# Optimization experiments

Hardware: AMD Instinct MI355X
Metric: run time of the kernel (lower is better)

## Reference

```python
import jax, jax.numpy as jnp
import numpy as np

NL, D, Di, N, R, K, V, NH = 24, 768, 1536, 16, 48, 4, 50280, 12
BATCH, SEQ = 4, 256


def setup_inputs():
    key = jax.random.key(0)
    it = iter(jax.random.split(key, 48))
    g = lambda shape, s=0.02: jax.random.normal(next(it), shape, jnp.float32) * s
    inp = {
        "question_ids": jax.random.randint(next(it), (BATCH, SEQ), 0, V),
        "question_mask": jnp.ones((BATCH, SEQ), jnp.int32),
        "answer_ids": jax.random.randint(next(it), (BATCH, SEQ), 0, V),
        "answer_mask": jnp.ones((BATCH, SEQ), jnp.int32),
        "embed": g((V, D)),
        "norm_w": jnp.ones((NL, D)),
        "in_proj_w": g((NL, 2 * Di, D)),
        "conv_w": g((NL, Di, K), 0.1),
        "conv_b": jnp.zeros((NL, Di)),
        "x_proj_w": g((NL, R + 2 * N, Di)),
        "dt_proj_w": g((NL, Di, R)),
        "dt_proj_b": g((NL, Di), 0.5) - 4.0,
        "A_log": jnp.log(jnp.broadcast_to(jnp.arange(1, N + 1, dtype=jnp.float32), (NL, Di, N))) + 0.0,
        "D_p": jnp.ones((NL, Di)),
        "out_proj_w": g((NL, D, Di)),
        "norm_f": jnp.ones((D,)),
        "ln1_w": jnp.ones((D,)), "ln1_b": jnp.zeros((D,)),
        "qkv_w": g((3 * D, D)), "qkv_b": jnp.zeros((3 * D,)),
        "attn_out_w": g((D, D)), "attn_out_b": jnp.zeros((D,)),
        "ln2_w": jnp.ones((D,)), "ln2_b": jnp.zeros((D,)),
        "ff1_w": g((4 * D, D)), "ff1_b": jnp.zeros((4 * D,)),
        "ff2_w": g((D, 4 * D)), "ff2_b": jnp.zeros((D,)),
        "C_w": g((1, N)), "proj_out_w": g((D, Di)),
        "B_w": g((N, 1)), "proj_in_w": g((Di, D), 0.002),
    }
    return inp


def _rms(x, w, eps=1e-5):
    return x * jax.lax.rsqrt(jnp.mean(x * x, axis=-1, keepdims=True) + eps) * w


def _ln(x, w, b, eps=1e-5):
    m = jnp.mean(x, axis=-1, keepdims=True)
    v = jnp.var(x, axis=-1, keepdims=True)
    return (x - m) * jax.lax.rsqrt(v + eps) * w + b


def _mamba_block(h, layer, init_state):
    nw, ipw, cw, cb, xpw, dpw, dpb, alog, dp, opw = layer
    x_in = _rms(h, nw)
    xz = jnp.einsum('bld,ed->ble', x_in, ipw)  # (B,L,2*Di)
    x, z = jnp.split(xz, 2, axis=-1)
    L = x.shape[1]
    xp = jnp.pad(x, ((0, 0), (K - 1, 0), (0, 0)))  # causal depthwise conv, kernel K
    x = sum(xp[:, k:k + L, :] * cw[:, k] for k in range(K)) + cb
    x = jax.nn.silu(x)
    dbl = jnp.einsum('bld,ed->ble', x, xpw)
    dt, Bm, Cm = dbl[..., :R], dbl[..., R:R + N], dbl[..., R + N:]
    delta = jax.nn.softplus(jnp.einsum('blr,dr->bld', dt, dpw) + dpb)  # (B,L,Di)
    A = -jnp.exp(alog)  # (Di,N)

    def step(hs, t):  # selective scan, carry (B,Di,N)
        d_t, x_t, B_t, C_t = t
        hs = jnp.exp(d_t[..., None] * A) * hs + (d_t * x_t)[..., None] * B_t[:, None, :]
        return hs, jnp.einsum('bdn,bn->bd', hs, C_t)

    xs = tuple(jnp.moveaxis(a, 1, 0) for a in (delta, x, Bm, Cm))
    last, ys = jax.lax.scan(step, init_state, xs)
    y = jnp.moveaxis(ys, 0, 1) + x * dp
    y = y * jax.nn.silu(z)
    return h + jnp.einsum('bld,od->blo', y, opw), last


def _backbone(ids, mask, embed, mamba_params, norm_f, init_states):
    h = embed[ids] * mask[..., None].astype(embed.dtype)
    block = jax.checkpoint(_mamba_block)  # remat per layer: bounds bwd memory

    def layer_step(carry, xs):
        *layer, st = xs
        return block(carry, tuple(layer), st)

    h, lasts = jax.lax.scan(layer_step, h, mamba_params + (init_states,))
    h = _rms(h, norm_f)
    return jnp.einsum('bld,vd->blv', h, embed), lasts  # tied lm head


def _tf_layer(x, ln1_w, ln1_b, qkv_w, qkv_b, attn_out_w, attn_out_b, ln2_w, ln2_b, ff1_w, ff1_b, ff2_w, ff2_b):
    B, S, _ = x.shape
    hd = D // NH
    y = _ln(x, ln1_w, ln1_b)  # norm_first pre-LN
    q, k, v = jnp.split(y @ qkv_w.T + qkv_b, 3, axis=-1)
    q = q.reshape(B, S, NH, hd); k = k.reshape(B, S, NH, hd); v = v.reshape(B, S, NH, hd)
    att = jax.nn.softmax(jnp.einsum('bqhd,bkhd->bhqk', q, k) / jnp.sqrt(jnp.float32(hd)), axis=-1)
    o = jnp.einsum('bhqk,bkhd->bqhd', att, v).reshape(B, S, D)
    x = x + o @ attn_out_w.T + attn_out_b
    y = _ln(x, ln2_w, ln2_b)
    return x + jax.nn.gelu(y @ ff1_w.T + ff1_b, approximate=False) @ ff2_w.T + ff2_b


def _refine(states, C_w, proj_out_w, B_w, proj_in_w, tf_params):
    # states: (B, NL, Di, N); 12-step recurrent state refinement
    for _ in range(12):
        d = jnp.einsum('bsdn,n->bsd', states, C_w[0])  # C: Linear(16,1), squeeze(-1)
        d = jnp.einsum('bsd,od->bso', d, proj_out_w)   # 1536 -> 768
        d = _tf_layer(d, *tf_params)
        d = jnp.einsum('bso,do->bsd', d, proj_in_w)    # 768 -> 1536
        states = states + d[..., None] * B_w[:, 0]     # B: Linear(1,16)
    return states


def reference(question_ids, question_mask, answer_ids, answer_mask, embed, norm_w, in_proj_w, conv_w, conv_b, x_proj_w, dt_proj_w, dt_proj_b, A_log, D_p, out_proj_w, norm_f, ln1_w, ln1_b, qkv_w, qkv_b, attn_out_w, attn_out_b, ln2_w, ln2_b, ff1_w, ff1_b, ff2_w, ff2_b, C_w, proj_out_w, B_w, proj_in_w):
    mamba_params = (norm_w, in_proj_w, conv_w, conv_b, x_proj_w, dt_proj_w, dt_proj_b, A_log, D_p, out_proj_w)
    tf_params = (ln1_w, ln1_b, qkv_w, qkv_b, attn_out_w, attn_out_b, ln2_w, ln2_b, ff1_w, ff1_b, ff2_w, ff2_b)
    Bsz = question_ids.shape[0]
    zeros = jnp.zeros((NL, Bsz, Di, N), embed.dtype)
    _, lasts = _backbone(question_ids, question_mask, embed, mamba_params, norm_f, zeros)
    states = jnp.moveaxis(lasts, 0, 1)  # torch.stack(states, dim=1): (B, NL, Di, N)
    states = _refine(states, C_w, proj_out_w, B_w, proj_in_w, tf_params)
    logits, _ = _backbone(answer_ids, answer_mask, embed, mamba_params, norm_f, jnp.moveaxis(states, 0, 1))
    return logits
```

## Files before the change

kernel.cpp:

```cpp
#include <hip/hip_runtime.h>
#include <math.h>

namespace {

constexpr int kNL = 24, kD = 768, kDi = 1536, kN = 16, kR = 48, kK = 4, kV = 50280, kNH = 12;
constexpr int kB = 4, kS = 256;
constexpr int kMtok = kB * kS;
constexpr int kMref = kB * kNL;
constexpr int kVp = 50304;
constexpr int kNx = 1568;
constexpr int kNxPad = 1600;

using bf16x8 = __attribute__((ext_vector_type(8))) short;
using f32x4  = __attribute__((ext_vector_type(4))) float;

__device__ __forceinline__ float siluf(float x) { return x / (1.f + __expf(-x)); }

__device__ __forceinline__ ushort f2b(float f) {
    union { float f; unsigned u; } v; v.f = f;
    unsigned u = v.u;
    unsigned r = (u + 0x7FFFu + ((u >> 16) & 1u)) >> 16;
    return (ushort)r;
}

#define GLOAD_LDS(g, l) \
    __builtin_amdgcn_global_load_lds((const __attribute__((address_space(1))) void*)(g), \
                                     (__attribute__((address_space(3))) void*)(l), 16, 0, 0)

template <int BM, int BN, int BIAS, int ACT, int RES, int OUTMODE, int PIPE>
__global__ __launch_bounds__(256, (PIPE == 3 ? 3 : 2)) void gemm_bf16(
    const ushort* __restrict__ A, int lda,
    const ushort* __restrict__ B, int ldb,
    float* __restrict__ C, int ldc,
    ushort* __restrict__ Cbf, int ldcb,
    float* __restrict__ C2,
    const float* __restrict__ bias,
    const float* __restrict__ aux,
    int M, int N, int K)
{
    constexpr int ACH = BM / 32;
    constexpr int BCH = BN / 32;
    constexpr int MI  = BM / 32;
    constexpr int NJ  = BN / 32;

    __shared__ ushort As[PIPE][BM * 64];
    __shared__ ushort Bs[PIPE][BN * 64];

    const int tid  = threadIdx.x;
    const int lane = tid & 63;
    const int wave = tid >> 6;
    const int m0 = blockIdx.y * BM;
    const int n0 = blockIdx.x * BN;
    const int wr = (wave >> 1) * (BM / 2);
    const int wc = (wave & 1) * (BN / 2);

    f32x4 acc[MI][NJ];
#pragma unroll
    for (int i = 0; i < MI; ++i)
#pragma unroll
        for (int j = 0; j < NJ; ++j) acc[i][j] = f32x4{0.f, 0.f, 0.f, 0.f};

    const int srow = lane >> 3;
    const int scol = ((lane & 7) ^ srow) * 8;
    const ushort* gA[ACH];
    const ushort* gB[BCH];
#pragma unroll
    for (int g = 0; g < ACH; ++g)
        gA[g] = A + (size_t)(m0 + (g * 4 + wave) * 8 + srow) * lda + scol;
#pragma unroll
    for (int g = 0; g < BCH; ++g)
        gB[g] = B + (size_t)(n0 + (g * 4 + wave) * 8 + srow) * ldb + scol;

    const int frow = lane & 15;
    const int kh   = lane >> 4;
    const int nt   = K >> 6;

    auto stage = [&](int t, int buf) {
        const int off = t * 64;
#pragma unroll
        for (int g = 0; g < ACH; ++g) GLOAD_LDS(gA[g] + off, &As[buf][(g * 4 + wave) * 512]);
#pragma unroll
        for (int g = 0; g < BCH; ++g) GLOAD_LDS(gB[g] + off, &Bs[buf][(g * 4 + wave) * 512]);
    };
    auto compute = [&](int buf) {
#pragma unroll
        for (int s = 0; s < 2; ++s) {
            bf16x8 fa[MI], fb[NJ];
#pragma unroll
            for (int i = 0; i < MI; ++i) {
                int r = wr + i * 16 + frow;
                int slot = (s * 4 + kh) ^ (r & 7);
                fa[i] = *(const bf16x8*)&As[buf][r * 64 + slot * 8];
            }
#pragma unroll
            for (int j = 0; j < NJ; ++j) {
                int r = wc + j * 16 + frow;
                int slot = (s * 4 + kh) ^ (r & 7);
                fb[j] = *(const bf16x8*)&Bs[buf][r * 64 + slot * 8];
            }
#pragma unroll
            for (int i = 0; i < MI; ++i)
#pragma unroll
                for (int j = 0; j < NJ; ++j)
                    acc[i][j] = __builtin_amdgcn_mfma_f32_16x16x32_bf16(fa[i], fb[j], acc[i][j], 0, 0, 0);
        }
    };

    if constexpr (PIPE == 3) {
        stage(0, 0);
        if (nt > 1) stage(1, 1);
        for (int t = 0; t < nt; ++t) {
            if (t < nt - 1) {
                asm volatile("s_waitcnt vmcnt(%0)" :: "n"(ACH + BCH) : "memory");
            } else {
                asm volatile("s_waitcnt vmcnt(0)" ::: "memory");
            }
            __builtin_amdgcn_s_barrier();
            if (t + 2 < nt) stage(t + 2, (t + 2) % 3);
            compute(t % 3);
        }
        __builtin_amdgcn_s_barrier();
    } else {
        stage(0, 0);
        __syncthreads();
        int cur = 0;
        for (int t = 0; t < nt; ++t) {
            if (t + 1 < nt) stage(t + 1, cur ^ 1);
            compute(cur);
            __syncthreads();
            cur ^= 1;
        }
    }

    const int ccol = lane & 15;
    const int crow = (lane >> 4) * 4;
#pragma unroll
    for (int i = 0; i < MI; ++i) {
#pragma unroll
        for (int j = 0; j < NJ; ++j) {
            int gn = n0 + wc + j * 16 + ccol;
            if (gn >= N) continue;
            float bv = BIAS ? bias[gn] : 0.f;
#pragma unroll
            for (int q = 0; q < 4; ++q) {
                int gm = m0 + wr + i * 16 + crow + q;
                if (gm >= M) continue;
                float v = acc[i][j][q] + bv;
                if (ACT == 1) v = fmaxf(v, 0.f) + log1pf(expf(-fabsf(v)));
                if (ACT == 2) v = 0.5f * v * (1.f + erff(v * 0.70710678118654752f));
                if (OUTMODE == 5) {
                    if (gn < kDi) C[(size_t)gm * kDi + gn] = v;
                    else C2[(size_t)(gn - kDi) * kMtok + gm] = siluf(v);
                } else if (OUTMODE == 6) {
                    if (gn < 32) C2[(size_t)gn * kMtok + gm] = v;
                    else {
                        float w = v + bias[gn - 32];
                        w = fmaxf(w, 0.f) + log1pf(expf(-fabsf(w)));
                        C[(size_t)(gn - 32) * kMtok + gm] = w;
                    }
                } else if (OUTMODE == 7) {
                    int bb = gm / kNL, ss = gm - bb * kNL;
                    float* stp = C2 + ((size_t)(ss * kB + bb) * kDi + gn) * kN;
                    float a2 = 0.f;
#pragma unroll
                    for (int nn = 0; nn < kN; ++nn) {
                        float sv = stp[nn] + v * bias[nn];
                        stp[nn] = sv;
                        a2 += sv * aux[nn];
                    }
                    Cbf[(size_t)gm * ldcb + gn] = f2b(a2);
                } else {
                    size_t ci = (size_t)gm * ldc + gn;
                    if (RES) v += C[ci];
                    if (OUTMODE != 2) C[ci] = v;
                    if (OUTMODE == 1 || OUTMODE == 2) Cbf[(size_t)gm * ldcb + gn] = f2b(v);
                }
            }
        }
    }
}

template <int BM, int BN, int BIAS, int ACT, int RES, int OUTMODE, int PIPE>
static void gemm(const ushort* A, int lda, const ushort* B, int ldb,
                 float* C, int ldc, ushort* Cb, int ldcb, float* C2,
                 const float* bias, const float* aux, int M, int N, int K, hipStream_t s)
{
    dim3 g((N + BN - 1) / BN, (M + BM - 1) / BM);
    gemm_bf16<BM, BN, BIAS, ACT, RES, OUTMODE, PIPE><<<g, dim3(256), 0, s>>>(
        A, lda, B, ldb, C, ldc, Cb, ldcb, C2, bias, aux, M, N, K);
}

__global__ void cvt_kernel(const float* __restrict__ src, ushort* __restrict__ dst, int n) {
    int i = (blockIdx.x * 256 + threadIdx.x) * 4;
    if (i >= n) return;
    float4 v = *(const float4*)(src + i);
    ushort4 o; o.x = f2b(v.x); o.y = f2b(v.y); o.z = f2b(v.z); o.w = f2b(v.w);
    *(ushort4*)(dst + i) = o;
}

__global__ void cvt_dpw_kernel(const float* __restrict__ src, ushort* __restrict__ dst) {
    int i = blockIdx.x * 256 + threadIdx.x;
    if (i >= 24 * 1536 * 64) return;
    int col = i & 63, row = i >> 6;
    dst[i] = (col < 48) ? f2b(src[(size_t)row * 48 + col]) : (ushort)0;
}

__global__ void cvt_xpwdtT_kernel(const float* __restrict__ src, ushort* __restrict__ dst) {
    int i = blockIdx.x * 256 + threadIdx.x;
    if (i >= 24 * 1536 * 64) return;
    int r = i & 63;
    int j = (i >> 6) % 1536;
    int l = i / (1536 * 64);
    dst[i] = (r < 48) ? f2b(src[((size_t)l * 80 + r) * 1536 + j]) : (ushort)0;
}

__global__ void cvt_bc_kernel(const float* __restrict__ src, ushort* __restrict__ dst) {
    int i = blockIdx.x * 256 + threadIdx.x;
    if (i >= 24 * 32 * 1536) return;
    int k = i % 1536;
    int gn = (i / 1536) % 32;
    int l = i / (32 * 1536);
    dst[((size_t)l * kNxPad + gn) * 1536 + k] = f2b(src[((size_t)l * 80 + 48 + gn) * 1536 + k]);
}

__global__ void embed_kernel(const int* __restrict__ ids, const int* __restrict__ msk,
                             const float* __restrict__ embed, float* __restrict__ h)
{
    int i = blockIdx.x * 256 + threadIdx.x;
    int row = i / kD, col = i - row * kD;
    h[i] = embed[(size_t)ids[row] * kD + col] * (float)msk[row];
}

__global__ __launch_bounds__(256) void rms_kernel(const float* __restrict__ x,
                                                  const float* __restrict__ w,
                                                  ushort* __restrict__ out)
{
    __shared__ float red[256];
    int row = blockIdx.x, tid = threadIdx.x;
    const float* xr = x + (size_t)row * kD;
    float s = 0.f;
    for (int j = tid; j < kD; j += 256) { float v = xr[j]; s += v * v; }
    red[tid] = s; __syncthreads();
    for (int o = 128; o > 0; o >>= 1) { if (tid < o) red[tid] += red[tid + o]; __syncthreads(); }
    float rs = rsqrtf(red[0] / (float)kD + 1e-5f);
    for (int j = tid; j < kD; j += 256) out[(size_t)row * kD + j] = f2b(xr[j] * rs * w[j]);
}

__global__ __launch_bounds__(256) void ln_kernel(const float* __restrict__ x,
                                                 const float* __restrict__ w,
                                                 const float* __restrict__ b,
                                                 ushort* __restrict__ out)
{
    __shared__ float r1[256], r2[256];
    int row = blockIdx.x, tid = threadIdx.x;
    const float* xr = x + (size_t)row * kD;
    float s = 0.f, s2 = 0.f;
    for (int j = tid; j < kD; j += 256) { float v = xr[j]; s += v; s2 += v * v; }
    r1[tid] = s; r2[tid] = s2; __syncthreads();
    for (int o = 128; o > 0; o >>= 1) {
        if (tid < o) { r1[tid] += r1[tid + o]; r2[tid] += r2[tid + o]; }
        __syncthreads();
    }
    float mean = r1[0] / (float)kD;
    float var = r2[0] / (float)kD - mean * mean;
    float rs = rsqrtf(var + 1e-5f);
    for (int j = tid; j < kD; j += 256)
        out[(size_t)row * kD + j] = f2b((xr[j] - mean) * rs * w[j] + b[j]);
}

__global__ __launch_bounds__(256) void conv_kernel(
    const float* __restrict__ xbuf, const float* __restrict__ cw,
    const float* __restrict__ cb, ushort* __restrict__ xc_bf,
    float* __restrict__ xcT)
{
    int d   = blockIdx.x * 256 + threadIdx.x;
    int bt0 = blockIdx.y * 16;
    int t0  = bt0 & (kS - 1);
    float w0 = cw[d * 4], w1 = cw[d * 4 + 1], w2 = cw[d * 4 + 2], w3 = cw[d * 4 + 3];
    float bias = cb[d];
    float xv[19];
#pragma unroll
    for (int j = 0; j < 19; ++j) {
        int tt = t0 - 3 + j;
        xv[j] = (tt >= 0) ? xbuf[(size_t)(bt0 - 3 + j) * kDi + d] : 0.f;
    }
    float out[16];
#pragma unroll
    for (int e = 0; e < 16; ++e) {
        float s = bias + xv[e] * w0 + xv[e + 1] * w1 + xv[e + 2] * w2 + xv[e + 3] * w3;
        float v = siluf(s);
        out[e] = v;
        xc_bf[(size_t)(bt0 + e) * kDi + d] = f2b(v);
    }
    float4* dst = (float4*)(xcT + (size_t)d * kMtok + bt0);
#pragma unroll
    for (int i = 0; i < 4; ++i)
        dst[i] = make_float4(out[i * 4], out[i * 4 + 1], out[i * 4 + 2], out[i * 4 + 3]);
}

__global__ __launch_bounds__(256) void scan_kernel(
    const float* __restrict__ dltT, const float* __restrict__ xcT,
    const float* __restrict__ zT, const float* __restrict__ bcT,
    const float* __restrict__ alog, const float* __restrict__ dp,
    float* __restrict__ states, ushort* __restrict__ y)
{
    int gid = blockIdx.x * 256 + threadIdx.x;
    int n = gid & 15;
    int d = (gid >> 4) % kDi;
    int b = gid / (kDi * kN);
    float Areg = -__expf(alog[d * kN + n]);
    float dpv = dp[d];
    size_t sidx = (size_t)(b * kDi + d) * kN + n;
    float hs = states[sidx];
    const float4* pD = (const float4*)(dltT + (size_t)d * kMtok + b * kS);
    const float4* pX = (const float4*)(xcT  + (size_t)d * kMtok + b * kS);
    const float4* pZ = (const float4*)(zT   + (size_t)d * kMtok + b * kS);
    const float4* pB = (const float4*)(bcT + (size_t)n * kMtok + b * kS);
    const float4* pC = (const float4*)(bcT + (size_t)(16 + n) * kMtok + b * kS);
    float4 D = pD[0], X = pX[0], Z = pZ[0], Bq = pB[0], Cq = pC[0];
    ushort* yrow = y + (size_t)(b * kS) * kDi + d;
    for (int g = 0; g < kS / 4; ++g) {
        float4 Dn, Xn, Zn, Bn, Cn;
        if (g + 1 < kS / 4) { Dn = pD[g + 1]; Xn = pX[g + 1]; Zn = pZ[g + 1]; Bn = pB[g + 1]; Cn = pC[g + 1]; }
#pragma unroll
        for (int e = 0; e < 4; ++e) {
            float dv = (&D.x)[e], xv = (&X.x)[e], zv = (&Z.x)[e];
            float Bv = (&Bq.x)[e], Cv = (&Cq.x)[e];
            hs = __expf(dv * Areg) * hs + (dv * xv) * Bv;
            float p = hs * Cv;
            p += __shfl_xor(p, 1, 16);
            p += __shfl_xor(p, 2, 16);
            p += __shfl_xor(p, 4, 16);
            p += __shfl_xor(p, 8, 16);
            if (n == 0) yrow[(size_t)(g * 4 + e) * kDi] = f2b((p + xv * dpv) * zv);
        }
        D = Dn; X = Xn; Z = Zn; Bq = Bn; Cq = Cn;
    }
    states[sidx] = hs;
}

__global__ void contract_kernel(const float* __restrict__ st, const float* __restrict__ Cw,
                                ushort* __restrict__ dDi)
{
    int i = blockIdx.x * 256 + threadIdx.x;
    int row = i / kDi, di = i - row * kDi;
    int b = row / kNL, s = row - b * kNL;
    const float* sp = st + ((size_t)(s * kB + b) * kDi + di) * kN;
    float acc = 0.f;
#pragma unroll
    for (int nn = 0; nn < kN; ++nn) acc += sp[nn] * Cw[nn];
    dDi[i] = f2b(acc);
}

__global__ __launch_bounds__(32) void attn_kernel(const float* __restrict__ qkv,
                                                  ushort* __restrict__ o)
{
    int b = blockIdx.x / kNH;
    int hh = blockIdx.x - b * kNH;
    int sq = threadIdx.x;
    if (sq >= kNL) return;
    const float* qrow = qkv + (size_t)(b * kNL + sq) * (3 * kD) + hh * 64;
    float q[64];
#pragma unroll
    for (int e = 0; e < 64; ++e) q[e] = qrow[e];
    float sc[kNL];
    float mx = -1e30f;
    for (int sk = 0; sk < kNL; ++sk) {
        const float* krow = qkv + (size_t)(b * kNL + sk) * (3 * kD) + kD + hh * 64;
        float dt = 0.f;
#pragma unroll
        for (int e = 0; e < 64; ++e) dt += q[e] * krow[e];
        dt *= 0.125f;
        sc[sk] = dt;
        mx = fmaxf(mx, dt);
    }
    float sum = 0.f;
    for (int sk = 0; sk < kNL; ++sk) { sc[sk] = expf(sc[sk] - mx); sum += sc[sk]; }
    float inv = 1.f / sum;
    float out[64];
#pragma unroll
    for (int e = 0; e < 64; ++e) out[e] = 0.f;
    for (int sk = 0; sk < kNL; ++sk) {
        float wgt = sc[sk] * inv;
        const float* vrow = qkv + (size_t)(b * kNL + sk) * (3 * kD) + 2 * kD + hh * 64;
#pragma unroll
        for (int e = 0; e < 64; ++e) out[e] += wgt * vrow[e];
    }
    ushort* orow = o + (size_t)(b * kNL + sq) * kD + hh * 64;
#pragma unroll
    for (int e = 0; e < 64; ++e) orow[e] = f2b(out[e]);
}

}

extern "C" void kernel_launch(void* const* d_in, const int* in_sizes, int n_in,
                              void* d_out, int out_size, void* d_ws, size_t ws_size,
                              hipStream_t stream)
{
    const int*   q_ids  = (const int*)d_in[0];
    const int*   q_msk  = (const int*)d_in[1];
    const int*   a_ids  = (const int*)d_in[2];
    const int*   a_msk  = (const int*)d_in[3];
    const float* embed  = (const float*)d_in[4];
    const float* norm_w = (const float*)d_in[5];
    const float* ipw    = (const float*)d_in[6];
    const float* cw     = (const float*)d_in[7];
    const float* cb     = (const float*)d_in[8];
    const float* xpw    = (const float*)d_in[9];
    const float* dpw    = (const float*)d_in[10];
    const float* dpb    = (const float*)d_in[11];
    const float* alog   = (const float*)d_in[12];
    const float* dpp    = (const float*)d_in[13];
    const float* opw    = (const float*)d_in[14];
    const float* norm_f = (const float*)d_in[15];
    const float* ln1w   = (const float*)d_in[16];
    const float* ln1b   = (const float*)d_in[17];
    const float* qkvw   = (const float*)d_in[18];
    const float* qkvbi  = (const float*)d_in[19];
    const float* aow    = (const float*)d_in[20];
    const float* aob    = (const float*)d_in[21];
    const float* ln2w   = (const float*)d_in[22];
    const float* ln2b   = (const float*)d_in[23];
    const float* ff1w   = (const float*)d_in[24];
    const float* ff1b   = (const float*)d_in[25];
    const float* ff2w   = (const float*)d_in[26];
    const float* ff2b   = (const float*)d_in[27];
    const float* Cwp    = (const float*)d_in[28];
    const float* powp   = (const float*)d_in[29];
    const float* Bwp    = (const float*)d_in[30];
    const float* piwp   = (const float*)d_in[31];

    char* base = (char*)d_ws;
    size_t cur = 0;
    auto allocB = [&](size_t bytes) { char* p = base + cur; cur = (cur + bytes + 255) & ~(size_t)255; return p; };
    auto allocF = [&](size_t n) { return (float*)allocB(n * 4); };
    auto allocH = [&](size_t n) { return (ushort*)allocB(n * 2); };

    float* h     = allocF((size_t)kMtok * kD);
    float* xbuf  = allocF((size_t)kMtok * kDi);
    float* zT    = allocF((size_t)kDi * kMtok);
    float* xcT   = allocF((size_t)kDi * kMtok);
    float* bcT   = allocF((size_t)32 * kMtok);
    float* dltT  = allocF((size_t)kDi * kMtok);
    float* st    = allocF((size_t)kNL * kB * kDi * kN);
    float* x768  = allocF((size_t)kMref * kD);
    float* qkvB  = allocF((size_t)kMref * 3 * kD);
    ushort* xin_bf  = allocH((size_t)kMtok * kD);
    ushort* xc_bf   = allocH((size_t)kMtok * kDi);
    ushort* yb_bf   = allocH((size_t)kMtok * kDi);
    ushort* dDi_bf  = allocH((size_t)128 * kDi);
    ushort* tb_bf   = allocH((size_t)128 * kD);
    ushort* o768_bf = allocH((size_t)128 * kD);
    ushort* f3_bf   = allocH((size_t)128 * 4 * kD);
    ushort* x768_bf = allocH((size_t)128 * kD);
    ushort* xpw2    = allocH((size_t)kNL * kNxPad * kDi);
    ushort* dpw_bf  = allocH((size_t)kNL * kDi * 64);
    ushort* xpwdtT  = allocH((size_t)kNL * kDi * 64);
    ushort* powp_bf = allocH((size_t)kD * kDi);
    ushort* qkvw_bf = allocH((size_t)3 * kD * kD);
    ushort* aow_bf  = allocH((size_t)kD * kD);
    ushort* ff1w_bf = allocH((size_t)4 * kD * kD);
    ushort* ff2w_bf = allocH((size_t)kD * 4 * kD);
    ushort* piw_bf  = allocH((size_t)kDi * kD);
    ushort* emb_bf  = allocH((size_t)kVp * kD);

    size_t base_end = cur;
    ushort* ipw_all = allocH((size_t)kNL * 2 * kDi * kD);
    ushort* opw_all = allocH((size_t)kNL * kD * kDi);
    bool full = (cur <= ws_size);
    ushort* ipw_stg = nullptr;
    ushort* opw_stg = nullptr;
    if (!full) {
        cur = base_end;
        ipw_stg = allocH((size_t)2 * kDi * kD);
        opw_stg = allocH((size_t)kD * kDi);
        if (cur > ws_size) return;
    }

    auto cvt = [&](const float* s, ushort* d, size_t n) {
        cvt_kernel<<<dim3((unsigned)((n / 4 + 255) / 256)), dim3(256), 0, stream>>>(s, d, (int)n);
    };

    hipMemsetAsync(st, 0, sizeof(float) * (size_t)kNL * kB * kDi * kN, stream);
    hipMemsetAsync(xpw2, 0, sizeof(ushort) * (size_t)kNL * kNxPad * kDi, stream);

    cvt_dpw_kernel<<<dim3(9216), dim3(256), 0, stream>>>(dpw, dpw_bf);
    cvt_xpwdtT_kernel<<<dim3(9216), dim3(256), 0, stream>>>(xpw, xpwdtT);
    cvt_bc_kernel<<<dim3(4608), dim3(256), 0, stream>>>(xpw, xpw2);
    for (int l = 0; l < kNL; ++l) {
        gemm<64, 64, 0, 0, 0, 2, 3>(dpw_bf + (size_t)l * kDi * 64, 64,
                                    xpwdtT + (size_t)l * kDi * 64, 64,
                                    nullptr, 0,
                                    xpw2 + (size_t)l * kNxPad * kDi + 32 * kDi, kDi,
                                    nullptr, nullptr, nullptr, kDi, kDi, 64, stream);
    }
    cvt(powp, powp_bf, (size_t)kD * kDi);
    cvt(qkvw, qkvw_bf, (size_t)3 * kD * kD);
    cvt(aow,  aow_bf,  (size_t)kD * kD);
    cvt(ff1w, ff1w_bf, (size_t)4 * kD * kD);
    cvt(ff2w, ff2w_bf, (size_t)kD * 4 * kD);
    cvt(piwp, piw_bf,  (size_t)kDi * kD);
    cvt(embed, emb_bf, (size_t)kV * kD);
    if (full) {
        cvt(ipw, ipw_all, (size_t)kNL * 2 * kDi * kD);
        cvt(opw, opw_all, (size_t)kNL * kD * kDi);
    }

    for (int pass = 0; pass < 2; ++pass) {
        const int* ids = pass ? a_ids : q_ids;
        const int* msk = pass ? a_msk : q_msk;

        embed_kernel<<<dim3(kMtok * kD / 256), dim3(256), 0, stream>>>(ids, msk, embed, h);

        for (int l = 0; l < kNL; ++l) {
            const ushort* ipw_l;
            const ushort* opw_l;
            if (full) {
                ipw_l = ipw_all + (size_t)l * 2 * kDi * kD;
                opw_l = opw_all + (size_t)l * kD * kDi;
            } else {
                cvt(ipw + (size_t)l * 2 * kDi * kD, ipw_stg, (size_t)2 * kDi * kD);
                cvt(opw + (size_t)l * kD * kDi, opw_stg, (size_t)kD * kDi);
                ipw_l = ipw_stg;
                opw_l = opw_stg;
            }
            rms_kernel<<<dim3(kMtok), dim3(256), 0, stream>>>(h, norm_w + (size_t)l * kD, xin_bf);
            gemm<64, 64, 0, 0, 0, 5, 3>(xin_bf, kD, ipw_l, kD, xbuf, kDi, nullptr, 0, zT,
                                        nullptr, nullptr, kMtok, 2 * kDi, kD, stream);
            conv_kernel<<<dim3(kDi / 256, kMtok / 16), dim3(256), 0, stream>>>(
                xbuf, cw + (size_t)l * kDi * kK, cb + (size_t)l * kDi, xc_bf, xcT);
            gemm<64, 64, 0, 0, 0, 6, 3>(xc_bf, kDi, xpw2 + (size_t)l * kNxPad * kDi, kDi,
                                        dltT, 0, nullptr, 0, bcT,
                                        dpb + (size_t)l * kDi, nullptr, kMtok, kNx, kDi, stream);
            scan_kernel<<<dim3(kB * kDi * kN / 256), dim3(256), 0, stream>>>(
                dltT, xcT, zT, bcT, alog + (size_t)l * kDi * kN, dpp + (size_t)l * kDi,
                st + (size_t)l * kB * kDi * kN, yb_bf);
            gemm<64, 64, 0, 0, 1, 0, 3>(yb_bf, kDi, opw_l, kDi, h, kD, nullptr, 0, nullptr,
                                        nullptr, nullptr, kMtok, kD, kDi, stream);
        }

        if (pass == 0) {
            contract_kernel<<<dim3(kMref * kDi / 256), dim3(256), 0, stream>>>(st, Cwp, dDi_bf);
            for (int it = 0; it < 12; ++it) {
                gemm<64, 64, 0, 0, 0, 0, 3>(dDi_bf, kDi, powp_bf, kDi, x768, kD, nullptr, 0, nullptr,
                                            nullptr, nullptr, kMref, kD, kDi, stream);
                ln_kernel<<<dim3(kMref), dim3(256), 0, stream>>>(x768, ln1w, ln1b, tb_bf);
                gemm<64, 64, 1, 0, 0, 0, 3>(tb_bf, kD, qkvw_bf, kD, qkvB, 3 * kD, nullptr, 0, nullptr,
                                            qkvbi, nullptr, kMref, 3 * kD, kD, stream);
                attn_kernel<<<dim3(kB * kNH), dim3(32), 0, stream>>>(qkvB, o768_bf);
                gemm<64, 64, 1, 0, 1, 0, 3>(o768_bf, kD, aow_bf, kD, x768, kD, nullptr, 0, nullptr,
                                            aob, nullptr, kMref, kD, kD, stream);
                ln_kernel<<<dim3(kMref), dim3(256), 0, stream>>>(x768, ln2w, ln2b, tb_bf);
                gemm<64, 64, 1, 2, 0, 2, 3>(tb_bf, kD, ff1w_bf, kD, nullptr, 0, f3_bf, 4 * kD, nullptr,
                                            ff1b, nullptr, kMref, 4 * kD, kD, stream);
                gemm<64, 64, 1, 0, 1, 1, 3>(f3_bf, 4 * kD, ff2w_bf, 4 * kD, x768, kD, x768_bf, kD, nullptr,
                                            ff2b, nullptr, kMref, kD, 4 * kD, stream);
                gemm<64, 64, 0, 0, 0, 7, 3>(x768_bf, kD, piw_bf, kD, nullptr, 0, dDi_bf, kDi, st,
                                            Bwp, Cwp, kMref, kDi, kD, stream);
            }
        } else {
            rms_kernel<<<dim3(kMtok), dim3(256), 0, stream>>>(h, norm_f, xin_bf);
            gemm<128, 128, 0, 0, 0, 0, 2>(xin_bf, kD, emb_bf, kD, (float*)d_out, kV, nullptr, 0, nullptr,
                                          nullptr, nullptr, kMtok, kV, kD, stream);
        }
    }
}
```

Baseline: 9.255 ms.

## Fuse RMSNorm into in_proj GEMM, unfold dt_proj, and store scan intermediates in bf16

```diff
diff --git a/kernel.cpp b/kernel.cpp
--- a/kernel.cpp
+++ b/kernel.cpp
@@ -8,11 +8,10 @@
 constexpr int kMtok = kB * kS;
 constexpr int kMref = kB * kNL;
 constexpr int kVp = 50304;
-constexpr int kNx = 1568;
-constexpr int kNxPad = 1600;
-
-using bf16x8 = __attribute__((ext_vector_type(8))) short;
-using f32x4  = __attribute__((ext_vector_type(4))) float;
+
+using bf16x8   = __attribute__((ext_vector_type(8))) short;
+using f32x4    = __attribute__((ext_vector_type(4))) float;
+using ushort8v = __attribute__((ext_vector_type(8))) unsigned short;
 
 __device__ __forceinline__ float siluf(float x) { return x / (1.f + __expf(-x)); }
 
@@ -22,12 +21,15 @@
     unsigned r = (u + 0x7FFFu + ((u >> 16) & 1u)) >> 16;
     return (ushort)r;
 }
+__device__ __forceinline__ float b2f(ushort u) {
+    union { unsigned u; float f; } v; v.u = (unsigned)u << 16; return v.f;
+}
 
 #define GLOAD_LDS(g, l) \
     __builtin_amdgcn_global_load_lds((const __attribute__((address_space(1))) void*)(g), \
                                      (__attribute__((address_space(3))) void*)(l), 16, 0, 0)
 
-template <int BM, int BN, int BIAS, int ACT, int RES, int OUTMODE, int PIPE>
+template <int BM, int BN, int BIAS, int ACT, int RES, int OUTMODE, int PIPE, int SSQ = 0>
 __global__ __launch_bounds__(256, (PIPE == 3 ? 3 : 2)) void gemm_bf16(
     const ushort* __restrict__ A, int lda,
     const ushort* __restrict__ B, int ldb,
@@ -134,6 +136,13 @@
 
     const int ccol = lane & 15;
     const int crow = (lane >> 4) * 4;
+    float rsq[MI][4];
+    if constexpr (SSQ) {
+#pragma unroll
+        for (int i = 0; i < MI; ++i)
+#pragma unroll
+            for (int q = 0; q < 4; ++q) rsq[i][q] = 0.f;
+    }
 #pragma unroll
     for (int i = 0; i < MI; ++i) {
 #pragma unroll
@@ -148,16 +157,12 @@
                 float v = acc[i][j][q] + bv;
                 if (ACT == 1) v = fmaxf(v, 0.f) + log1pf(expf(-fabsf(v)));
                 if (ACT == 2) v = 0.5f * v * (1.f + erff(v * 0.70710678118654752f));
-                if (OUTMODE == 5) {
-                    if (gn < kDi) C[(size_t)gm * kDi + gn] = v;
-                    else C2[(size_t)(gn - kDi) * kMtok + gm] = siluf(v);
-                } else if (OUTMODE == 6) {
-                    if (gn < 32) C2[(size_t)gn * kMtok + gm] = v;
-                    else {
-                        float w = v + bias[gn - 32];
-                        w = fmaxf(w, 0.f) + log1pf(expf(-fabsf(w)));
-                        C[(size_t)(gn - 32) * kMtok + gm] = w;
-                    }
+                if (OUTMODE == 3) {
+                    if (gn < 48) Cbf[(size_t)gm * 64 + gn] = f2b(v);
+                    else if (gn < 64) { Cbf[(size_t)gm * 64 + gn] = 0; C2[(size_t)(gn - 48) * kMtok + gm] = v; }
+                    else if (gn < 80) C2[(size_t)(gn - 48) * kMtok + gm] = v;
+                } else if (OUTMODE == 4) {
+                    ((ushort*)C2)[(size_t)gn * kMtok + gm] = f2b(v);
                 } else if (OUTMODE == 7) {
                     int bb = gm / kNL, ss = gm - bb * kNL;
                     float* stp = C2 + ((size_t)(ss * kB + bb) * kDi + gn) * kN;
@@ -174,20 +179,176 @@
                     if (RES) v += C[ci];
                     if (OUTMODE != 2) C[ci] = v;
                     if (OUTMODE == 1 || OUTMODE == 2) Cbf[(size_t)gm * ldcb + gn] = f2b(v);
+                    if constexpr (SSQ) rsq[i][q] += v * v;
                 }
             }
         }
     }
-}
-
-template <int BM, int BN, int BIAS, int ACT, int RES, int OUTMODE, int PIPE>
+    if constexpr (SSQ) {
+#pragma unroll
+        for (int i = 0; i < MI; ++i)
+#pragma unroll
+            for (int q = 0; q < 4; ++q) {
+                rsq[i][q] += __shfl_xor(rsq[i][q], 1, 16);
+                rsq[i][q] += __shfl_xor(rsq[i][q], 2, 16);
+                rsq[i][q] += __shfl_xor(rsq[i][q], 4, 16);
+                rsq[i][q] += __shfl_xor(rsq[i][q], 8, 16);
+            }
+        float* red = (float*)&As[0][0];
+        __syncthreads();
+        if ((lane & 15) == 0) {
+#pragma unroll
+            for (int i = 0; i < MI; ++i)
+#pragma unroll
+                for (int q = 0; q < 4; ++q) {
+                    int rl = (wave >> 1) * 32 + i * 16 + (lane >> 4) * 4 + q;
+                    red[(wave & 1) * 64 + rl] = rsq[i][q];
+                }
+        }
+        __syncthreads();
+        if (tid < 64) C2[(size_t)blockIdx.x * kMtok + m0 + tid] = red[tid] + red[64 + tid];
+    }
+}
+
+template <int BM, int BN, int BIAS, int ACT, int RES, int OUTMODE, int PIPE, int SSQ = 0>
 static void gemm(const ushort* A, int lda, const ushort* B, int ldb,
                  float* C, int ldc, ushort* Cb, int ldcb, float* C2,
                  const float* bias, const float* aux, int M, int N, int K, hipStream_t s)
 {
     dim3 g((N + BN - 1) / BN, (M + BM - 1) / BM);
-    gemm_bf16<BM, BN, BIAS, ACT, RES, OUTMODE, PIPE><<<g, dim3(256), 0, s>>>(
+    gemm_bf16<BM, BN, BIAS, ACT, RES, OUTMODE, PIPE, SSQ><<<g, dim3(256), 0, s>>>(
         A, lda, B, ldb, C, ldc, Cb, ldcb, C2, bias, aux, M, N, K);
+}
+
+__global__ __launch_bounds__(256, 4) void gemm_rms(
+    const float* __restrict__ hbuf, const float* __restrict__ ssq,
+    const float* __restrict__ nw,
+    const ushort* __restrict__ B, int ldb,
+    ushort* __restrict__ Xbf, ushort* __restrict__ zTb,
+    int M, int N, int K)
+{
+    constexpr int MI = 2, NJ = 2, BCH = 2;
+    __shared__ ushort As[2][64 * 64];
+    __shared__ ushort Bs[2][64 * 64];
+    const int tid  = threadIdx.x;
+    const int lane = tid & 63;
+    const int wave = tid >> 6;
+    const int m0 = blockIdx.y * 64;
+    const int n0 = blockIdx.x * 64;
+    const int wr = (wave >> 1) * 32;
+    const int wc = (wave & 1) * 32;
+
+    f32x4 acc[MI][NJ];
+#pragma unroll
+    for (int i = 0; i < MI; ++i)
+#pragma unroll
+        for (int j = 0; j < NJ; ++j) acc[i][j] = f32x4{0.f, 0.f, 0.f, 0.f};
+
+    const int srow = lane >> 3;
+    const int scol = ((lane & 7) ^ srow) * 8;
+    const ushort* gB[BCH];
+#pragma unroll
+    for (int g = 0; g < BCH; ++g)
+        gB[g] = B + (size_t)(n0 + (g * 4 + wave) * 8 + srow) * ldb + scol;
+
+    int arow[2];
+    float rs[2];
+#pragma unroll
+    for (int g = 0; g < 2; ++g) {
+        arow[g] = m0 + (g * 4 + wave) * 8 + srow;
+        float s = 0.f;
+#pragma unroll
+        for (int c = 0; c < 12; ++c) s += ssq[c * kMtok + arow[g]];
+        rs[g] = rsqrtf(s * (1.f / 768.f) + 1e-5f);
+    }
+
+    const int frow = lane & 15;
+    const int kh   = lane >> 4;
+    const int nt   = K >> 6;
+
+    float4 av[2][2], wv[2];
+    auto loadA = [&](int t) {
+        int k = t * 64 + scol;
+        wv[0] = *(const float4*)&nw[k];
+        wv[1] = *(const float4*)&nw[k + 4];
+#pragma unroll
+        for (int g = 0; g < 2; ++g) {
+            av[g][0] = *(const float4*)&hbuf[(size_t)arow[g] * K + k];
+            av[g][1] = *(const float4*)&hbuf[(size_t)arow[g] * K + k + 4];
+        }
+    };
+    auto writeA = [&](int buf) {
+#pragma unroll
+        for (int g = 0; g < 2; ++g) {
+            ushort8v o;
+            o[0] = f2b(av[g][0].x * rs[g] * wv[0].x);
+            o[1] = f2b(av[g][0].y * rs[g] * wv[0].y);
+            o[2] = f2b(av[g][0].z * rs[g] * wv[0].z);
+            o[3] = f2b(av[g][0].w * rs[g] * wv[0].w);
+            o[4] = f2b(av[g][1].x * rs[g] * wv[1].x);
+            o[5] = f2b(av[g][1].y * rs[g] * wv[1].y);
+            o[6] = f2b(av[g][1].z * rs[g] * wv[1].z);
+            o[7] = f2b(av[g][1].w * rs[g] * wv[1].w);
+            *(ushort8v*)&As[buf][(g * 4 + wave) * 512 + lane * 8] = o;
+        }
+    };
+    auto stageB = [&](int t, int buf) {
+#pragma unroll
+        for (int g = 0; g < BCH; ++g) GLOAD_LDS(gB[g] + t * 64, &Bs[buf][(g * 4 + wave) * 512]);
+    };
+    auto compute = [&](int buf) {
+#pragma unroll
+        for (int s = 0; s < 2; ++s) {
+            bf16x8 fa[MI], fb[NJ];
+#pragma unroll
+            for (int i = 0; i < MI; ++i) {
+                int r = wr + i * 16 + frow;
+                int slot = (s * 4 + kh) ^ (r & 7);
+                fa[i] = *(const bf16x8*)&As[buf][r * 64 + slot * 8];
+            }
+#pragma unroll
+            for (int j = 0; j < NJ; ++j) {
+                int r = wc + j * 16 + frow;
+                int slot = (s * 4 + kh) ^ (r & 7);
+                fb[j] = *(const bf16x8*)&Bs[buf][r * 64 + slot * 8];
+            }
+#pragma unroll
+            for (int i = 0; i < MI; ++i)
+#pragma unroll
+                for (int j = 0; j < NJ; ++j)
+                    acc[i][j] = __builtin_amdgcn_mfma_f32_16x16x32_bf16(fa[i], fb[j], acc[i][j], 0, 0, 0);
+        }
+    };
+
+    loadA(0);
+    stageB(0, 0);
+    writeA(0);
+    __syncthreads();
+    int cur = 0;
+    for (int t = 0; t < nt; ++t) {
+        if (t + 1 < nt) { loadA(t + 1); stageB(t + 1, cur ^ 1); }
+        compute(cur);
+        if (t + 1 < nt) writeA(cur ^ 1);
+        __syncthreads();
+        cur ^= 1;
+    }
+
+    const int ccol = lane & 15;
+    const int crow = (lane >> 4) * 4;
+#pragma unroll
+    for (int i = 0; i < MI; ++i) {
+#pragma unroll
+        for (int j = 0; j < NJ; ++j) {
+            int gn = n0 + wc + j * 16 + ccol;
+#pragma unroll
+            for (int q = 0; q < 4; ++q) {
+                int gm = m0 + wr + i * 16 + crow + q;
+                float v = acc[i][j][q];
+                if (gn < kDi) Xbf[(size_t)gm * kDi + gn] = f2b(v);
+                else zTb[(size_t)(gn - kDi) * kMtok + gm] = f2b(siluf(v));
+            }
+        }
+    }
 }
 
 __global__ void cvt_kernel(const float* __restrict__ src, ushort* __restrict__ dst, int n) {
@@ -198,6 +359,16 @@
     *(ushort4*)(dst + i) = o;
 }
 
+__global__ void cvt_xpw_kernel(const float* __restrict__ src, ushort* __restrict__ dst) {
+    int i = (blockIdx.x * 256 + threadIdx.x) * 4;
+    if (i >= 24 * 80 * 1536) return;
+    int l = i / (80 * 1536), r = i - l * (80 * 1536);
+    int row = r / 1536, col = r - row * 1536;
+    float4 v = *(const float4*)(src + i);
+    ushort4 o; o.x = f2b(v.x); o.y = f2b(v.y); o.z = f2b(v.z); o.w = f2b(v.w);
+    *(ushort4*)(dst + ((size_t)(l * 128 + row)) * 1536 + col) = o;
+}
+
 __global__ void cvt_dpw_kernel(const float* __restrict__ src, ushort* __restrict__ dst) {
     int i = blockIdx.x * 256 + threadIdx.x;
     if (i >= 24 * 1536 * 64) return;
@@ -205,30 +376,18 @@
     dst[i] = (col < 48) ? f2b(src[(size_t)row * 48 + col]) : (ushort)0;
 }
 
-__global__ void cvt_xpwdtT_kernel(const float* __restrict__ src, ushort* __restrict__ dst) {
-    int i = blockIdx.x * 256 + threadIdx.x;
-    if (i >= 24 * 1536 * 64) return;
-    int r = i & 63;
-    int j = (i >> 6) % 1536;
-    int l = i / (1536 * 64);
-    dst[i] = (r < 48) ? f2b(src[((size_t)l * 80 + r) * 1536 + j]) : (ushort)0;
-}
-
-__global__ void cvt_bc_kernel(const float* __restrict__ src, ushort* __restrict__ dst) {
-    int i = blockIdx.x * 256 + threadIdx.x;
-    if (i >= 24 * 32 * 1536) return;
-    int k = i % 1536;
-    int gn = (i / 1536) % 32;
-    int l = i / (32 * 1536);
-    dst[((size_t)l * kNxPad + gn) * 1536 + k] = f2b(src[((size_t)l * 80 + 48 + gn) * 1536 + k]);
-}
-
 __global__ void embed_kernel(const int* __restrict__ ids, const int* __restrict__ msk,
-                             const float* __restrict__ embed, float* __restrict__ h)
+                             const float* __restrict__ embed, float* __restrict__ h,
+                             float* __restrict__ ssq)
 {
     int i = blockIdx.x * 256 + threadIdx.x;
     int row = i / kD, col = i - row * kD;
-    h[i] = embed[(size_t)ids[row] * kD + col] * (float)msk[row];
+    float v = embed[(size_t)ids[row] * kD + col] * (float)msk[row];
+    h[i] = v;
+    float s = v * v;
+    s += __shfl_xor(s, 1);  s += __shfl_xor(s, 2);  s += __shfl_xor(s, 4);
+    s += __shfl_xor(s, 8);  s += __shfl_xor(s, 16); s += __shfl_xor(s, 32);
+    if ((threadIdx.x & 63) == 0) ssq[(col >> 6) * kMtok + row] = s;
 }
 
 __global__ __launch_bounds__(256) void rms_kernel(const float* __restrict__ x,
@@ -263,15 +422,15 @@
     }
     float mean = r1[0] / (float)kD;
     float var = r2[0] / (float)kD - mean * mean;
-    float rs = rsqrtf(var + 1e-5f);
+    float rsv = rsqrtf(var + 1e-5f);
     for (int j = tid; j < kD; j += 256)
-        out[(size_t)row * kD + j] = f2b((xr[j] - mean) * rs * w[j] + b[j]);
+        out[(size_t)row * kD + j] = f2b((xr[j] - mean) * rsv * w[j] + b[j]);
 }
 
 __global__ __launch_bounds__(256) void conv_kernel(
-    const float* __restrict__ xbuf, const float* __restrict__ cw,
+    const ushort* __restrict__ xb, const float* __restrict__ cw,
     const float* __restrict__ cb, ushort* __restrict__ xc_bf,
-    float* __restrict__ xcT)
+    ushort* __restrict__ xcT)
 {
     int d   = blockIdx.x * 256 + threadIdx.x;
     int bt0 = blockIdx.y * 16;
@@ -282,25 +441,23 @@
 #pragma unroll
     for (int j = 0; j < 19; ++j) {
         int tt = t0 - 3 + j;
-        xv[j] = (tt >= 0) ? xbuf[(size_t)(bt0 - 3 + j) * kDi + d] : 0.f;
-    }
-    float out[16];
+        xv[j] = (tt >= 0) ? b2f(xb[(size_t)(bt0 - 3 + j) * kDi + d]) : 0.f;
+    }
+    ushort8v o0, o1;
 #pragma unroll
     for (int e = 0; e < 16; ++e) {
         float s = bias + xv[e] * w0 + xv[e + 1] * w1 + xv[e + 2] * w2 + xv[e + 3] * w3;
-        float v = siluf(s);
-        out[e] = v;
-        xc_bf[(size_t)(bt0 + e) * kDi + d] = f2b(v);
-    }
-    float4* dst = (float4*)(xcT + (size_t)d * kMtok + bt0);
-#pragma unroll
-    for (int i = 0; i < 4; ++i)
-        dst[i] = make_float4(out[i * 4], out[i * 4 + 1], out[i * 4 + 2], out[i * 4 + 3]);
+        ushort us = f2b(siluf(s));
+        xc_bf[(size_t)(bt0 + e) * kDi + d] = us;
+        if (e < 8) o0[e] = us; else o1[e - 8] = us;
+    }
+    *(ushort8v*)(xcT + (size_t)d * kMtok + bt0)     = o0;
+    *(ushort8v*)(xcT + (size_t)d * kMtok + bt0 + 8) = o1;
 }
 
 __global__ __launch_bounds__(256) void scan_kernel(
-    const float* __restrict__ dltT, const float* __restrict__ xcT,
-    const float* __restrict__ zT, const float* __restrict__ bcT,
+    const ushort* __restrict__ dltT, const ushort* __restrict__ xcT,
+    const ushort* __restrict__ zT, const float* __restrict__ bcT,
     const float* __restrict__ alog, const float* __restrict__ dp,
     float* __restrict__ states, ushort* __restrict__ y)
 {
@@ -312,29 +469,35 @@
     float dpv = dp[d];
     size_t sidx = (size_t)(b * kDi + d) * kN + n;
     float hs = states[sidx];
-    const float4* pD = (const float4*)(dltT + (size_t)d * kMtok + b * kS);
-    const float4* pX = (const float4*)(xcT  + (size_t)d * kMtok + b * kS);
-    const float4* pZ = (const float4*)(zT   + (size_t)d * kMtok + b * kS);
+    const ushort8v* pD = (const ushort8v*)(dltT + (size_t)d * kMtok + b * kS);
+    const ushort8v* pX = (const ushort8v*)(xcT  + (size_t)d * kMtok + b * kS);
+    const ushort8v* pZ = (const ushort8v*)(zT   + (size_t)d * kMtok + b * kS);
     const float4* pB = (const float4*)(bcT + (size_t)n * kMtok + b * kS);
     const float4* pC = (const float4*)(bcT + (size_t)(16 + n) * kMtok + b * kS);
-    float4 D = pD[0], X = pX[0], Z = pZ[0], Bq = pB[0], Cq = pC[0];
+    ushort8v D = pD[0], X = pX[0], Z = pZ[0];
+    float4 B0 = pB[0], B1 = pB[1], C0 = pC[0], C1 = pC[1];
     ushort* yrow = y + (size_t)(b * kS) * kDi + d;
-    for (int g = 0; g < kS / 4; ++g) {
-        float4 Dn, Xn, Zn, Bn, Cn;
-        if (g + 1 < kS / 4) { Dn = pD[g + 1]; Xn = pX[g + 1]; Zn = pZ[g + 1]; Bn = pB[g + 1]; Cn = pC[g + 1]; }
-#pragma unroll
-        for (int e = 0; e < 4; ++e) {
-            float dv = (&D.x)[e], xv = (&X.x)[e], zv = (&Z.x)[e];
-            float Bv = (&Bq.x)[e], Cv = (&Cq.x)[e];
+    for (int g = 0; g < kS / 8; ++g) {
+        ushort8v Dn, Xn, Zn; float4 Bn0, Bn1, Cn0, Cn1;
+        if (g + 1 < kS / 8) {
+            Dn = pD[g + 1]; Xn = pX[g + 1]; Zn = pZ[g + 1];
+            Bn0 = pB[2 * g + 2]; Bn1 = pB[2 * g + 3];
+            Cn0 = pC[2 * g + 2]; Cn1 = pC[2 * g + 3];
+        }
+#pragma unroll
+        for (int e = 0; e < 8; ++e) {
+            float dv = b2f(D[e]), xv = b2f(X[e]), zv = b2f(Z[e]);
+            float Bv = (e < 4) ? (&B0.x)[e] : (&B1.x)[e - 4];
+            float Cv = (e < 4) ? (&C0.x)[e] : (&C1.x)[e - 4];
             hs = __expf(dv * Areg) * hs + (dv * xv) * Bv;
             float p = hs * Cv;
             p += __shfl_xor(p, 1, 16);
             p += __shfl_xor(p, 2, 16);
             p += __shfl_xor(p, 4, 16);
             p += __shfl_xor(p, 8, 16);
-            if (n == 0) yrow[(size_t)(g * 4 + e) * kDi] = f2b((p + xv * dpv) * zv);
-        }
-        D = Dn; X = Xn; Z = Zn; Bq = Bn; Cq = Cn;
+            if (n == 0) yrow[(size_t)(g * 8 + e) * kDi] = f2b((p + xv * dpv) * zv);
+        }
+        D = Dn; X = Xn; Z = Zn; B0 = Bn0; B1 = Bn1; C0 = Cn0; C1 = Cn1;
     }
     states[sidx] = hs;
 }
@@ -437,25 +600,26 @@
     auto allocH = [&](size_t n) { return (ushort*)allocB(n * 2); };
 
     float* h     = allocF((size_t)kMtok * kD);
-    float* xbuf  = allocF((size_t)kMtok * kDi);
-    float* zT    = allocF((size_t)kDi * kMtok);
-    float* xcT   = allocF((size_t)kDi * kMtok);
+    float* ssqp  = allocF((size_t)12 * kMtok);
     float* bcT   = allocF((size_t)32 * kMtok);
-    float* dltT  = allocF((size_t)kDi * kMtok);
     float* st    = allocF((size_t)kNL * kB * kDi * kN);
     float* x768  = allocF((size_t)kMref * kD);
     float* qkvB  = allocF((size_t)kMref * 3 * kD);
+    ushort* x_bf    = allocH((size_t)kMtok * kDi);
+    ushort* zT_b    = allocH((size_t)kDi * kMtok);
+    ushort* xcT_b   = allocH((size_t)kDi * kMtok);
+    ushort* dltT_b  = allocH((size_t)kDi * kMtok);
+    ushort* xc_bf   = allocH((size_t)kMtok * kDi);
+    ushort* dtin_bf = allocH((size_t)kMtok * 64);
+    ushort* yb_bf   = allocH((size_t)kMtok * kDi);
     ushort* xin_bf  = allocH((size_t)kMtok * kD);
-    ushort* xc_bf   = allocH((size_t)kMtok * kDi);
-    ushort* yb_bf   = allocH((size_t)kMtok * kDi);
     ushort* dDi_bf  = allocH((size_t)128 * kDi);
     ushort* tb_bf   = allocH((size_t)128 * kD);
     ushort* o768_bf = allocH((size_t)128 * kD);
     ushort* f3_bf   = allocH((size_t)128 * 4 * kD);
     ushort* x768_bf = allocH((size_t)128 * kD);
-    ushort* xpw2    = allocH((size_t)kNL * kNxPad * kDi);
+    ushort* xpw_bf  = allocH((size_t)kNL * 128 * kDi);
     ushort* dpw_bf  = allocH((size_t)kNL * kDi * 64);
-    ushort* xpwdtT  = allocH((size_t)kNL * kDi * 64);
     ushort* powp_bf = allocH((size_t)kD * kDi);
     ushort* qkvw_bf = allocH((size_t)3 * kD * kD);
     ushort* aow_bf  = allocH((size_t)kD * kD);
@@ -482,18 +646,9 @@
     };
 
     hipMemsetAsync(st, 0, sizeof(float) * (size_t)kNL * kB * kDi * kN, stream);
-    hipMemsetAsync(xpw2, 0, sizeof(ushort) * (size_t)kNL * kNxPad * kDi, stream);
-
+
+    cvt_xpw_kernel<<<dim3(2880), dim3(256), 0, stream>>>(xpw, xpw_bf);
     cvt_dpw_kernel<<<dim3(9216), dim3(256), 0, stream>>>(dpw, dpw_bf);
-    cvt_xpwdtT_kernel<<<dim3(9216), dim3(256), 0, stream>>>(xpw, xpwdtT);
-    cvt_bc_kernel<<<dim3(4608), dim3(256), 0, stream>>>(xpw, xpw2);
-    for (int l = 0; l < kNL; ++l) {
-        gemm<64, 64, 0, 0, 0, 2, 3>(dpw_bf + (size_t)l * kDi * 64, 64,
-                                    xpwdtT + (size_t)l * kDi * 64, 64,
-                                    nullptr, 0,
-                                    xpw2 + (size_t)l * kNxPad * kDi + 32 * kDi, kDi,
-                                    nullptr, nullptr, nullptr, kDi, kDi, 64, stream);
-    }
     cvt(powp, powp_bf, (size_t)kD * kDi);
     cvt(qkvw, qkvw_bf, (size_t)3 * kD * kD);
     cvt(aow,  aow_bf,  (size_t)kD * kD);
@@ -510,7 +665,7 @@
         const int* ids = pass ? a_ids : q_ids;
         const int* msk = pass ? a_msk : q_msk;
 
-        embed_kernel<<<dim3(kMtok * kD / 256), dim3(256), 0, stream>>>(ids, msk, embed, h);
+        embed_kernel<<<dim3(kMtok * kD / 256), dim3(256), 0, stream>>>(ids, msk, embed, h, ssqp);
 
         for (int l = 0; l < kNL; ++l) {
             const ushort* ipw_l;
@@ -524,19 +679,21 @@
                 ipw_l = ipw_stg;
                 opw_l = opw_stg;
             }
-            rms_kernel<<<dim3(kMtok), dim3(256), 0, stream>>>(h, norm_w + (size_t)l * kD, xin_bf);
-            gemm<64, 64, 0, 0, 0, 5, 3>(xin_bf, kD, ipw_l, kD, xbuf, kDi, nullptr, 0, zT,
-                                        nullptr, nullptr, kMtok, 2 * kDi, kD, stream);
+            gemm_rms<<<dim3(48, 16), dim3(256), 0, stream>>>(
+                h, ssqp, norm_w + (size_t)l * kD, ipw_l, kD, x_bf, zT_b, kMtok, 2 * kDi, kD);
             conv_kernel<<<dim3(kDi / 256, kMtok / 16), dim3(256), 0, stream>>>(
-                xbuf, cw + (size_t)l * kDi * kK, cb + (size_t)l * kDi, xc_bf, xcT);
-            gemm<64, 64, 0, 0, 0, 6, 3>(xc_bf, kDi, xpw2 + (size_t)l * kNxPad * kDi, kDi,
-                                        dltT, 0, nullptr, 0, bcT,
-                                        dpb + (size_t)l * kDi, nullptr, kMtok, kNx, kDi, stream);
+                x_bf, cw + (size_t)l * kDi * kK, cb + (size_t)l * kDi, xc_bf, xcT_b);
+            gemm<64, 64, 0, 0, 0, 3, 3>(xc_bf, kDi, xpw_bf + (size_t)l * 128 * kDi, kDi,
+                                        nullptr, 0, dtin_bf, 0, bcT,
+                                        nullptr, nullptr, kMtok, 128, kDi, stream);
+            gemm<64, 64, 1, 1, 0, 4, 3>(dtin_bf, 64, dpw_bf + (size_t)l * kDi * 64, 64,
+                                        nullptr, 0, nullptr, 0, (float*)dltT_b,
+                                        dpb + (size_t)l * kDi, nullptr, kMtok, kDi, 64, stream);
             scan_kernel<<<dim3(kB * kDi * kN / 256), dim3(256), 0, stream>>>(
-                dltT, xcT, zT, bcT, alog + (size_t)l * kDi * kN, dpp + (size_t)l * kDi,
+                dltT_b, xcT_b, zT_b, bcT, alog + (size_t)l * kDi * kN, dpp + (size_t)l * kDi,
                 st + (size_t)l * kB * kDi * kN, yb_bf);
-            gemm<64, 64, 0, 0, 1, 0, 3>(yb_bf, kDi, opw_l, kDi, h, kD, nullptr, 0, nullptr,
-                                        nullptr, nullptr, kMtok, kD, kDi, stream);
+            gemm<64, 64, 0, 0, 1, 0, 3, 1>(yb_bf, kDi, opw_l, kDi, h, kD, nullptr, 0, ssqp,
+                                           nullptr, nullptr, kMtok, kD, kDi, stream);
         }
 
         if (pass == 0) {
```

New measurement: 8.637 ms. 6.7% less time.
